# Kernel optimization log

Hardware: AMD Instinct MI355X
Metric: run time of the kernel (lower is better)

The kernel has to match this reference:

```python
import jax, jax.numpy as jnp
import numpy as np
from jax import lax

FH, FW = 5, 5  # filter_width, filter_height


def setup_inputs() -> dict:
    key = jax.random.key(0)
    k_in, k_f, k_b = jax.random.split(key, 3)
    return {
        "input": jax.random.normal(k_in, (8192, 8192), dtype=jnp.float32),
        "filter": jax.random.normal(k_f, (FH, FW), dtype=jnp.float32),
        "bias": jax.random.normal(k_b, (1, 1), dtype=jnp.float32),
    }


def reference(input, filter, bias):
    # Splat conv: out[i+di, j+dj] += input[i,j] * filter[di,dj]
    # == TRUE convolution with FULL padding -> output (H+FH-1, W+FW-1).
    # lax.conv does cross-correlation, so flip the filter in both spatial dims.
    fh, fw = filter.shape
    x = input[None, None]                      # NCHW, [1,1,H,W]
    k = jnp.flip(filter, (0, 1))[None, None]   # OIHW, [1,1,fh,fw]
    out = lax.conv_general_dilated(
        x, k,
        window_strides=(1, 1),
        padding=[(fh - 1, fh - 1), (fw - 1, fw - 1)],
        dimension_numbers=("NCHW", "OIHW", "NCHW"),
    )
    # Note: the original forward does NOT add bias (bias is only saved for bwd).
    return out[0, 0]
```

## Files before the change

kernel.cpp:

```cpp
#include <hip/hip_runtime.h>


#define IN_H 8192
#define IN_W 8192
#define OUT_H 8196
#define OUT_W 8196
#define NG 2049
#define NRG 2049

__global__ __launch_bounds__(256, 4) void splat_conv_kernel(
    const float* __restrict__ in, const float* __restrict__ flt,
    float* __restrict__ out) {
  const int g = blockIdx.x * 64 + threadIdx.x;
  const int rg = blockIdx.y * 4 + threadIdx.y;
  if (g >= NG || rg >= NRG) return;

  float f[25];
#pragma unroll
  for (int i = 0; i < 25; ++i) f[i] = flt[i];

  const int orow = rg * 4;
  const int c0 = 4 * g - 4;

  float acc[4][4];
#pragma unroll
  for (int k = 0; k < 4; ++k)
#pragma unroll
    for (int m = 0; m < 4; ++m) acc[k][m] = 0.f;

  const bool interior = (g >= 1) & (g <= NG - 2) & (rg >= 1) & (rg <= 2047);

  float4 A[8], B[8];
  if (interior) {
    const float* rp = in + (size_t)(orow - 4) * IN_W + c0;
#pragma unroll
    for (int rr = 0; rr < 8; ++rr) {
      A[rr] = *(const float4*)(rp);
      B[rr] = *(const float4*)(rp + 4);
      rp += IN_W;
    }
  } else {
    const bool lo_ok = (g != 0);
    const bool hi_ok = (g != NG - 1);
#pragma unroll
    for (int rr = 0; rr < 8; ++rr) {
      const int r = orow - 4 + rr;
      A[rr] = make_float4(0.f, 0.f, 0.f, 0.f);
      B[rr] = make_float4(0.f, 0.f, 0.f, 0.f);
      if (r >= 0 && r < IN_H) {
        const float* rp = in + (size_t)r * IN_W + c0;
        if (lo_ok) A[rr] = *(const float4*)(rp);
        if (hi_ok) B[rr] = *(const float4*)(rp + 4);
      }
    }
  }

#pragma unroll
  for (int rr = 0; rr < 8; ++rr) {
    float x[8];
    x[0] = A[rr].x; x[1] = A[rr].y; x[2] = A[rr].z; x[3] = A[rr].w;
    x[4] = B[rr].x; x[5] = B[rr].y; x[6] = B[rr].z; x[7] = B[rr].w;
#pragma unroll
    for (int k = 0; k < 4; ++k) {
      const int di = k + 4 - rr;
      if (di < 0 || di > 4) continue;
#pragma unroll
      for (int dj = 0; dj < 5; ++dj) {
        const float w = f[di * 5 + dj];
#pragma unroll
        for (int m = 0; m < 4; ++m) acc[k][m] += x[m + 4 - dj] * w;
      }
    }
  }

  float* op = out + (size_t)orow * OUT_W + 4 * g;
#pragma unroll
  for (int k = 0; k < 4; ++k) {
    *(float4*)(op) = make_float4(acc[k][0], acc[k][1], acc[k][2], acc[k][3]);
    op += OUT_W;
  }
}

extern "C" void kernel_launch(void* const* d_in, const int* in_sizes, int n_in,
                              void* d_out, int out_size, void* d_ws,
                              size_t ws_size, hipStream_t stream) {
  const float* in = (const float*)d_in[0];
  const float* flt = (const float*)d_in[1];
  float* out = (float*)d_out;

  dim3 block(64, 4);
  dim3 grid((NG + 63) / 64, (NRG + 3) / 4);
  splat_conv_kernel<<<grid, block, 0, stream>>>(in, flt, out);
}
```

Before: 457.5 us.

## Stream each thread down a 16-row-group strip with sliding input window

Each thread now handles a vertical strip of 16 output row-groups and keeps an 8-row sliding window of input in registers. Each step loads only 4 new rows, where the old code reloaded 8 rows per output tile, which halves redundant global/L2 input reads. Filter weights are forced into scalar registers via readfirstlane. The cost is a smaller grid with fewer waves and a loop-carried dependency, so there is less latency hiding and less parallelism.

```diff
diff --git a/kernel.cpp b/kernel.cpp
--- a/kernel.cpp
+++ b/kernel.cpp
@@ -7,77 +7,161 @@
 #define OUT_W 8196
 #define NG 2049
 #define NRG 2049
+#define SPAN 16
+
+__device__ __forceinline__ float sgpr_f32(float v) {
+  return __int_as_float(__builtin_amdgcn_readfirstlane(__float_as_int(v)));
+}
 
 __global__ __launch_bounds__(256, 4) void splat_conv_kernel(
     const float* __restrict__ in, const float* __restrict__ flt,
     float* __restrict__ out) {
   const int g = blockIdx.x * 64 + threadIdx.x;
-  const int rg = blockIdx.y * 4 + threadIdx.y;
-  if (g >= NG || rg >= NRG) return;
+  if (g >= NG) return;
+  const int strip = blockIdx.y * 4 + threadIdx.y;
+  const int rg0 = strip * SPAN;
+  if (rg0 >= NRG) return;
+  const int rg1 = (rg0 + SPAN < NRG) ? rg0 + SPAN : NRG;
 
   float f[25];
 #pragma unroll
-  for (int i = 0; i < 25; ++i) f[i] = flt[i];
+  for (int i = 0; i < 25; ++i) f[i] = sgpr_f32(flt[i]);
 
-  const int orow = rg * 4;
   const int c0 = 4 * g - 4;
+  const bool col_int = (g >= 1) & (g <= NG - 2);
+  const bool rows_ok = (rg0 >= 1) & (rg1 - 1 <= 2047);
 
-  float acc[4][4];
+  if (col_int & rows_ok) {
+    const float* rp = in + (size_t)(4 * rg0 - 4) * IN_W + c0;
+    float4 W[8][2];
 #pragma unroll
-  for (int k = 0; k < 4; ++k)
+    for (int r = 0; r < 8; ++r) {
+      W[r][0] = *(const float4*)(rp);
+      W[r][1] = *(const float4*)(rp + 4);
+      rp += IN_W;
+    }
+    float* op = out + (size_t)(4 * rg0) * OUT_W + 4 * g;
+
+#pragma unroll 2
+    for (int rg = rg0; rg < rg1 - 1; ++rg) {
+      float4 P[4][2];
 #pragma unroll
-    for (int m = 0; m < 4; ++m) acc[k][m] = 0.f;
-
-  const bool interior = (g >= 1) & (g <= NG - 2) & (rg >= 1) & (rg <= 2047);
-
-  float4 A[8], B[8];
-  if (interior) {
-    const float* rp = in + (size_t)(orow - 4) * IN_W + c0;
+      for (int r = 0; r < 4; ++r) {
+        P[r][0] = *(const float4*)(rp);
+        P[r][1] = *(const float4*)(rp + 4);
+        rp += IN_W;
+      }
+      float acc[4][4];
 #pragma unroll
-    for (int rr = 0; rr < 8; ++rr) {
-      A[rr] = *(const float4*)(rp);
-      B[rr] = *(const float4*)(rp + 4);
-      rp += IN_W;
+      for (int k = 0; k < 4; ++k)
+#pragma unroll
+        for (int m = 0; m < 4; ++m) acc[k][m] = 0.f;
+#pragma unroll
+      for (int rr = 0; rr < 8; ++rr) {
+        float x[8];
+        x[0] = W[rr][0].x; x[1] = W[rr][0].y; x[2] = W[rr][0].z; x[3] = W[rr][0].w;
+        x[4] = W[rr][1].x; x[5] = W[rr][1].y; x[6] = W[rr][1].z; x[7] = W[rr][1].w;
+#pragma unroll
+        for (int k = 0; k < 4; ++k) {
+          const int di = k + 4 - rr;
+          if (di < 0 || di > 4) continue;
+#pragma unroll
+          for (int dj = 0; dj < 5; ++dj) {
+            const float w = f[di * 5 + dj];
+#pragma unroll
+            for (int m = 0; m < 4; ++m) acc[k][m] += x[m + 4 - dj] * w;
+          }
+        }
+      }
+      float* o = op;
+#pragma unroll
+      for (int k = 0; k < 4; ++k) {
+        *(float4*)(o) = make_float4(acc[k][0], acc[k][1], acc[k][2], acc[k][3]);
+        o += OUT_W;
+      }
+      op += 4 * OUT_W;
+#pragma unroll
+      for (int r = 0; r < 4; ++r) {
+        W[r][0] = W[r + 4][0]; W[r][1] = W[r + 4][1];
+        W[r + 4][0] = P[r][0]; W[r + 4][1] = P[r][1];
+      }
+    }
+    {
+      float acc[4][4];
+#pragma unroll
+      for (int k = 0; k < 4; ++k)
+#pragma unroll
+        for (int m = 0; m < 4; ++m) acc[k][m] = 0.f;
+#pragma unroll
+      for (int rr = 0; rr < 8; ++rr) {
+        float x[8];
+        x[0] = W[rr][0].x; x[1] = W[rr][0].y; x[2] = W[rr][0].z; x[3] = W[rr][0].w;
+        x[4] = W[rr][1].x; x[5] = W[rr][1].y; x[6] = W[rr][1].z; x[7] = W[rr][1].w;
+#pragma unroll
+        for (int k = 0; k < 4; ++k) {
+          const int di = k + 4 - rr;
+          if (di < 0 || di > 4) continue;
+#pragma unroll
+          for (int dj = 0; dj < 5; ++dj) {
+            const float w = f[di * 5 + dj];
+#pragma unroll
+            for (int m = 0; m < 4; ++m) acc[k][m] += x[m + 4 - dj] * w;
+          }
+        }
+      }
+      float* o = op;
+#pragma unroll
+      for (int k = 0; k < 4; ++k) {
+        *(float4*)(o) = make_float4(acc[k][0], acc[k][1], acc[k][2], acc[k][3]);
+        o += OUT_W;
+      }
     }
   } else {
     const bool lo_ok = (g != 0);
     const bool hi_ok = (g != NG - 1);
+    for (int rg = rg0; rg < rg1; ++rg) {
+      const int orow = rg * 4;
+      float4 A[8], B[8];
 #pragma unroll
-    for (int rr = 0; rr < 8; ++rr) {
-      const int r = orow - 4 + rr;
-      A[rr] = make_float4(0.f, 0.f, 0.f, 0.f);
-      B[rr] = make_float4(0.f, 0.f, 0.f, 0.f);
-      if (r >= 0 && r < IN_H) {
-        const float* rp = in + (size_t)r * IN_W + c0;
-        if (lo_ok) A[rr] = *(const float4*)(rp);
-        if (hi_ok) B[rr] = *(const float4*)(rp + 4);
+      for (int rr = 0; rr < 8; ++rr) {
+        const int r = orow - 4 + rr;
+        A[rr] = make_float4(0.f, 0.f, 0.f, 0.f);
+        B[rr] = make_float4(0.f, 0.f, 0.f, 0.f);
+        if (r >= 0 && r < IN_H) {
+          const float* rp = in + (size_t)r * IN_W + c0;
+          if (lo_ok) A[rr] = *(const float4*)(rp);
+          if (hi_ok) B[rr] = *(const float4*)(rp + 4);
+        }
+      }
+      float acc[4][4];
+#pragma unroll
+      for (int k = 0; k < 4; ++k)
+#pragma unroll
+        for (int m = 0; m < 4; ++m) acc[k][m] = 0.f;
+#pragma unroll
+      for (int rr = 0; rr < 8; ++rr) {
+        float x[8];
+        x[0] = A[rr].x; x[1] = A[rr].y; x[2] = A[rr].z; x[3] = A[rr].w;
+        x[4] = B[rr].x; x[5] = B[rr].y; x[6] = B[rr].z; x[7] = B[rr].w;
+#pragma unroll
+        for (int k = 0; k < 4; ++k) {
+          const int di = k + 4 - rr;
+          if (di < 0 || di > 4) continue;
+#pragma unroll
+          for (int dj = 0; dj < 5; ++dj) {
+            const float w = f[di * 5 + dj];
+#pragma unroll
+            for (int m = 0; m < 4; ++m) acc[k][m] += x[m + 4 - dj] * w;
+          }
+        }
+      }
+      float* o = out + (size_t)orow * OUT_W + 4 * g;
+#pragma unroll
+      for (int k = 0; k < 4; ++k) {
+        *(float4*)(o) = make_float4(acc[k][0], acc[k][1], acc[k][2], acc[k][3]);
+        o += OUT_W;
       }
     }
-  }
-
-#pragma unroll
-  for (int rr = 0; rr < 8; ++rr) {
-    float x[8];
-    x[0] = A[rr].x; x[1] = A[rr].y; x[2] = A[rr].z; x[3] = A[rr].w;
-    x[4] = B[rr].x; x[5] = B[rr].y; x[6] = B[rr].z; x[7] = B[rr].w;
-#pragma unroll
-    for (int k = 0; k < 4; ++k) {
-      const int di = k + 4 - rr;
-      if (di < 0 || di > 4) continue;
-#pragma unroll
-      for (int dj = 0; dj < 5; ++dj) {
-        const float w = f[di * 5 + dj];
-#pragma unroll
-        for (int m = 0; m < 4; ++m) acc[k][m] += x[m + 4 - dj] * w;
-      }
-    }
-  }
-
-  float* op = out + (size_t)orow * OUT_W + 4 * g;
-#pragma unroll
-  for (int k = 0; k < 4; ++k) {
-    *(float4*)(op) = make_float4(acc[k][0], acc[k][1], acc[k][2], acc[k][3]);
-    op += OUT_W;
   }
 }
 
@@ -88,7 +172,8 @@
   const float* flt = (const float*)d_in[1];
   float* out = (float*)d_out;
 
+  const int nstrips = (NRG + SPAN - 1) / SPAN;
   dim3 block(64, 4);
-  dim3 grid((NG + 63) / 64, (NRG + 3) / 4);
+  dim3 grid((NG + 63) / 64, (nstrips + 3) / 4);
   splat_conv_kernel<<<grid, block, 0, stream>>>(in, flt, out);
 }
```

New measurement: 592.6 us. 29.5% more time.

## Process vertical strips per thread with rolling register window for row reuse

Applied to the files above, without the earlier changes.

Each thread now computes 16 consecutive 4x4 output row-groups, keeping a sliding 8-row input window in registers so each new group loads only 4 fresh rows instead of 8. Filter weights are broadcast into scalar registers via readfirstlane. This targets redundant input loads, but reduces the grid size by 16x and raises per-thread register pressure, which may limit latency hiding and parallelism.

```diff
diff --git a/kernel.cpp b/kernel.cpp
--- a/kernel.cpp
+++ b/kernel.cpp
@@ -7,77 +7,160 @@
 #define OUT_W 8196
 #define NG 2049
 #define NRG 2049
+#define SPAN 16
+
+__device__ __forceinline__ float sgpr_f32(float v) {
+  return __int_as_float(__builtin_amdgcn_readfirstlane(__float_as_int(v)));
+}
+
+#define CONTRIB(RR, SA, SB)                                               \
+  do {                                                                    \
+    float x[8];                                                           \
+    x[0] = (SA).x; x[1] = (SA).y; x[2] = (SA).z; x[3] = (SA).w;           \
+    x[4] = (SB).x; x[5] = (SB).y; x[6] = (SB).z; x[7] = (SB).w;           \
+    _Pragma("unroll") for (int k = 0; k < 4; ++k) {                       \
+      const int di = k + 4 - (RR);                                        \
+      if (di >= 0 && di <= 4) {                                           \
+        _Pragma("unroll") for (int dj = 0; dj < 5; ++dj) {                \
+          const float w = f[di * 5 + dj];                                 \
+          _Pragma("unroll") for (int m = 0; m < 4; ++m)                   \
+              acc[k][m] += x[m + 4 - dj] * w;                             \
+        }                                                                 \
+      }                                                                   \
+    }                                                                     \
+  } while (0)
+
+#define BODY(S0a, S0b, S1a, S1b, S2a, S2b, S3a, S3b,                      \
+             S4a, S4b, S5a, S5b, S6a, S6b, S7a, S7b)                      \
+  do {                                                                    \
+    float acc[4][4] = {{0.f}};                                            \
+    CONTRIB(0, S0a, S0b);                                                 \
+    CONTRIB(1, S1a, S1b);                                                 \
+    CONTRIB(2, S2a, S2b);                                                 \
+    CONTRIB(3, S3a, S3b);                                                 \
+    S0a = *(const float4*)(rp); S0b = *(const float4*)(rp + 4); rp += IN_W; \
+    S1a = *(const float4*)(rp); S1b = *(const float4*)(rp + 4); rp += IN_W; \
+    S2a = *(const float4*)(rp); S2b = *(const float4*)(rp + 4); rp += IN_W; \
+    S3a = *(const float4*)(rp); S3b = *(const float4*)(rp + 4); rp += IN_W; \
+    CONTRIB(4, S4a, S4b);                                                 \
+    CONTRIB(5, S5a, S5b);                                                 \
+    CONTRIB(6, S6a, S6b);                                                 \
+    CONTRIB(7, S7a, S7b);                                                 \
+    *(float4*)(op) = make_float4(acc[0][0], acc[0][1], acc[0][2], acc[0][3]); \
+    *(float4*)(op + OUT_W) = make_float4(acc[1][0], acc[1][1], acc[1][2], acc[1][3]); \
+    *(float4*)(op + 2 * OUT_W) = make_float4(acc[2][0], acc[2][1], acc[2][2], acc[2][3]); \
+    *(float4*)(op + 3 * OUT_W) = make_float4(acc[3][0], acc[3][1], acc[3][2], acc[3][3]); \
+    op += 4 * OUT_W;                                                      \
+  } while (0)
+
+#define FINAL(S0a, S0b, S1a, S1b, S2a, S2b, S3a, S3b,                     \
+              S4a, S4b, S5a, S5b, S6a, S6b, S7a, S7b)                     \
+  do {                                                                    \
+    float acc[4][4] = {{0.f}};                                            \
+    CONTRIB(0, S0a, S0b);                                                 \
+    CONTRIB(1, S1a, S1b);                                                 \
+    CONTRIB(2, S2a, S2b);                                                 \
+    CONTRIB(3, S3a, S3b);                                                 \
+    CONTRIB(4, S4a, S4b);                                                 \
+    CONTRIB(5, S5a, S5b);                                                 \
+    CONTRIB(6, S6a, S6b);                                                 \
+    CONTRIB(7, S7a, S7b);                                                 \
+    *(float4*)(op) = make_float4(acc[0][0], acc[0][1], acc[0][2], acc[0][3]); \
+    *(float4*)(op + OUT_W) = make_float4(acc[1][0], acc[1][1], acc[1][2], acc[1][3]); \
+    *(float4*)(op + 2 * OUT_W) = make_float4(acc[2][0], acc[2][1], acc[2][2], acc[2][3]); \
+    *(float4*)(op + 3 * OUT_W) = make_float4(acc[3][0], acc[3][1], acc[3][2], acc[3][3]); \
+  } while (0)
 
 __global__ __launch_bounds__(256, 4) void splat_conv_kernel(
     const float* __restrict__ in, const float* __restrict__ flt,
     float* __restrict__ out) {
   const int g = blockIdx.x * 64 + threadIdx.x;
-  const int rg = blockIdx.y * 4 + threadIdx.y;
-  if (g >= NG || rg >= NRG) return;
+  if (g >= NG) return;
+  const int strip = blockIdx.y * 4 + threadIdx.y;
+  const int rg0 = strip * SPAN;
+  if (rg0 >= NRG) return;
+  const int rg1 = (rg0 + SPAN < NRG) ? rg0 + SPAN : NRG;
 
   float f[25];
 #pragma unroll
-  for (int i = 0; i < 25; ++i) f[i] = flt[i];
+  for (int i = 0; i < 25; ++i) f[i] = sgpr_f32(flt[i]);
 
-  const int orow = rg * 4;
   const int c0 = 4 * g - 4;
+  const bool col_int = (g >= 1) & (g <= NG - 2);
+  const bool rows_ok = (rg0 >= 1) & (rg1 == rg0 + SPAN) & (rg1 - 1 <= 2047);
 
-  float acc[4][4];
-#pragma unroll
-  for (int k = 0; k < 4; ++k)
-#pragma unroll
-    for (int m = 0; m < 4; ++m) acc[k][m] = 0.f;
+  if (col_int & rows_ok) {
+    const float* rp = in + (size_t)(4 * rg0 - 4) * IN_W + c0;
+    float* op = out + (size_t)(4 * rg0) * OUT_W + 4 * g;
 
-  const bool interior = (g >= 1) & (g <= NG - 2) & (rg >= 1) & (rg <= 2047);
+    float4 W0a, W0b, W1a, W1b, W2a, W2b, W3a, W3b;
+    float4 W4a, W4b, W5a, W5b, W6a, W6b, W7a, W7b;
+    W0a = *(const float4*)(rp); W0b = *(const float4*)(rp + 4); rp += IN_W;
+    W1a = *(const float4*)(rp); W1b = *(const float4*)(rp + 4); rp += IN_W;
+    W2a = *(const float4*)(rp); W2b = *(const float4*)(rp + 4); rp += IN_W;
+    W3a = *(const float4*)(rp); W3b = *(const float4*)(rp + 4); rp += IN_W;
+    W4a = *(const float4*)(rp); W4b = *(const float4*)(rp + 4); rp += IN_W;
+    W5a = *(const float4*)(rp); W5b = *(const float4*)(rp + 4); rp += IN_W;
+    W6a = *(const float4*)(rp); W6b = *(const float4*)(rp + 4); rp += IN_W;
+    W7a = *(const float4*)(rp); W7b = *(const float4*)(rp + 4); rp += IN_W;
 
-  float4 A[8], B[8];
-  if (interior) {
-    const float* rp = in + (size_t)(orow - 4) * IN_W + c0;
-#pragma unroll
-    for (int rr = 0; rr < 8; ++rr) {
-      A[rr] = *(const float4*)(rp);
-      B[rr] = *(const float4*)(rp + 4);
-      rp += IN_W;
+#pragma unroll 1
+    for (int p = 0; p < 7; ++p) {
+      BODY(W0a, W0b, W1a, W1b, W2a, W2b, W3a, W3b,
+           W4a, W4b, W5a, W5b, W6a, W6b, W7a, W7b);
+      BODY(W4a, W4b, W5a, W5b, W6a, W6b, W7a, W7b,
+           W0a, W0b, W1a, W1b, W2a, W2b, W3a, W3b);
     }
+    BODY(W0a, W0b, W1a, W1b, W2a, W2b, W3a, W3b,
+         W4a, W4b, W5a, W5b, W6a, W6b, W7a, W7b);
+    FINAL(W4a, W4b, W5a, W5b, W6a, W6b, W7a, W7b,
+          W0a, W0b, W1a, W1b, W2a, W2b, W3a, W3b);
   } else {
     const bool lo_ok = (g != 0);
     const bool hi_ok = (g != NG - 1);
+    for (int rg = rg0; rg < rg1; ++rg) {
+      const int orow = rg * 4;
+      float4 A[8], B[8];
 #pragma unroll
-    for (int rr = 0; rr < 8; ++rr) {
-      const int r = orow - 4 + rr;
-      A[rr] = make_float4(0.f, 0.f, 0.f, 0.f);
-      B[rr] = make_float4(0.f, 0.f, 0.f, 0.f);
-      if (r >= 0 && r < IN_H) {
-        const float* rp = in + (size_t)r * IN_W + c0;
-        if (lo_ok) A[rr] = *(const float4*)(rp);
-        if (hi_ok) B[rr] = *(const float4*)(rp + 4);
+      for (int rr = 0; rr < 8; ++rr) {
+        const int r = orow - 4 + rr;
+        A[rr] = make_float4(0.f, 0.f, 0.f, 0.f);
+        B[rr] = make_float4(0.f, 0.f, 0.f, 0.f);
+        if (r >= 0 && r < IN_H) {
+          const float* rp = in + (size_t)r * IN_W + c0;
+          if (lo_ok) A[rr] = *(const float4*)(rp);
+          if (hi_ok) B[rr] = *(const float4*)(rp + 4);
+        }
+      }
+      float acc[4][4];
+#pragma unroll
+      for (int k = 0; k < 4; ++k)
+#pragma unroll
+        for (int m = 0; m < 4; ++m) acc[k][m] = 0.f;
+#pragma unroll
+      for (int rr = 0; rr < 8; ++rr) {
+        float x[8];
+        x[0] = A[rr].x; x[1] = A[rr].y; x[2] = A[rr].z; x[3] = A[rr].w;
+        x[4] = B[rr].x; x[5] = B[rr].y; x[6] = B[rr].z; x[7] = B[rr].w;
+#pragma unroll
+        for (int k = 0; k < 4; ++k) {
+          const int di = k + 4 - rr;
+          if (di < 0 || di > 4) continue;
+#pragma unroll
+          for (int dj = 0; dj < 5; ++dj) {
+            const float w = f[di * 5 + dj];
+#pragma unroll
+            for (int m = 0; m < 4; ++m) acc[k][m] += x[m + 4 - dj] * w;
+          }
+        }
+      }
+      float* o = out + (size_t)orow * OUT_W + 4 * g;
+#pragma unroll
+      for (int k = 0; k < 4; ++k) {
+        *(float4*)(o) = make_float4(acc[k][0], acc[k][1], acc[k][2], acc[k][3]);
+        o += OUT_W;
       }
     }
-  }
-
-#pragma unroll
-  for (int rr = 0; rr < 8; ++rr) {
-    float x[8];
-    x[0] = A[rr].x; x[1] = A[rr].y; x[2] = A[rr].z; x[3] = A[rr].w;
-    x[4] = B[rr].x; x[5] = B[rr].y; x[6] = B[rr].z; x[7] = B[rr].w;
-#pragma unroll
-    for (int k = 0; k < 4; ++k) {
-      const int di = k + 4 - rr;
-      if (di < 0 || di > 4) continue;
-#pragma unroll
-      for (int dj = 0; dj < 5; ++dj) {
-        const float w = f[di * 5 + dj];
-#pragma unroll
-        for (int m = 0; m < 4; ++m) acc[k][m] += x[m + 4 - dj] * w;
-      }
-    }
-  }
-
-  float* op = out + (size_t)orow * OUT_W + 4 * g;
-#pragma unroll
-  for (int k = 0; k < 4; ++k) {
-    *(float4*)(op) = make_float4(acc[k][0], acc[k][1], acc[k][2], acc[k][3]);
-    op += OUT_W;
   }
 }
 
@@ -88,7 +171,8 @@
   const float* flt = (const float*)d_in[1];
   float* out = (float*)d_out;
 
+  const int nstrips = (NRG + SPAN - 1) / SPAN;
   dim3 block(64, 4);
-  dim3 grid((NG + 63) / 64, (NRG + 3) / 4);
+  dim3 grid((NG + 63) / 64, (nstrips + 3) / 4);
   splat_conv_kernel<<<grid, block, 0, stream>>>(in, flt, out);
 }
```

Result: slower. 748.2 us (+63.5%).
